# Performance work log

Measured on AMD Instinct MI355X. Metric: run time of the kernel, lower is better.

Reference implementation:

```python
import jax, jax.numpy as jnp
import numpy as np

B = 2097152   # batch
Z = 16        # z_dim
K = 64        # num_hidden_nodes


def setup_inputs() -> dict:
    key = jax.random.key(0)
    k1, k2, k3, k4, k5 = jax.random.split(key, 5)
    return {
        "z": jax.random.normal(k1, (B, Z), dtype=jnp.float32),
        "a_0": jax.random.normal(k2, (1,), dtype=jnp.float32),
        "bk": jax.random.normal(k3, (K,), dtype=jnp.float32),
        "ck": jax.random.normal(k4, (K, Z), dtype=jnp.float32),
        "dk": jax.random.normal(k5, (K,), dtype=jnp.float32),
    }


def reference(z, a_0, bk, ck, dk):
    # Vectorized over the batch: y[b] = a_0 + sum_k bk[k] * tanh((ck @ z[b])[k] + dk[k])
    h = jnp.tanh(jnp.einsum("bz,kz->bk", z, ck) + dk)  # [B, K]
    y = a_0 + h @ bk                                     # [B]
    return y[:, None]                                     # [B, 1]
```

## Files before the change

kernel.cpp:

```cpp
#include <hip/hip_runtime.h>
#include <stdint.h>

typedef __attribute__((ext_vector_type(8)))  short  short8;
typedef __attribute__((ext_vector_type(8)))  __bf16 bf16x8;
typedef __attribute__((ext_vector_type(16))) float  floatx16;
typedef __attribute__((ext_vector_type(4)))  float  floatx4;
typedef __attribute__((ext_vector_type(2)))  float  float2v;
typedef __attribute__((ext_vector_type(4)))  uint32_t uint4v;

union Frag { short8 s; bf16x8 v; uint4v d; };
union FU   { float f; uint32_t u; };

__device__ __forceinline__ short f2bf(float f) {
    FU x; x.f = f;
    uint32_t r = x.u + 0x7fffu + ((x.u >> 16) & 1u);
    return (short)(r >> 16);
}

__device__ __forceinline__ uint32_t pack_bf2(float lo, float hi) {
    FU a, b; a.f = lo; b.f = hi;
    return __builtin_amdgcn_perm(b.u + 0x8000u, a.u + 0x8000u, 0x07060302u);
}

__device__ __forceinline__ float fexp2(float x) { return __builtin_amdgcn_exp2f(x); }
__device__ __forceinline__ float frcp(float x)  { return __builtin_amdgcn_rcpf(x); }
__device__ __forceinline__ float fclamp(float x, float lo, float hi) {
#if __has_builtin(__builtin_amdgcn_fmed3f)
    return __builtin_amdgcn_fmed3f(x, lo, hi);
#else
    return fminf(fmaxf(x, lo), hi);
#endif
}

__device__ __forceinline__ float2v tpair(float a, float b) {
    float2v t;
    t.x = fexp2(fclamp(a, -30.0f, 30.0f));
    t.y = fexp2(fclamp(b, -30.0f, 30.0f));
    return t + 1.0f;
}

__global__ __launch_bounds__(256) void mave_kernel(
    const float* __restrict__ z,
    const float* __restrict__ a0,
    const float* __restrict__ bk,
    const float* __restrict__ ck,
    const float* __restrict__ dk,
    float* __restrict__ out,
    int ntiles)
{
    const int lane = threadIdx.x & 63;
    const int m    = lane & 31;
    const int g    = lane >> 5;
    const float S  = 2.885390081777927f;

    const int wid   = (int)((blockIdx.x * blockDim.x + threadIdx.x) >> 6);
    const int tile0 = wid * 8;
    if (tile0 >= ntiles) return;
    const int tlast = ntiles - 1;

    const float* zp = z + (size_t)m * 16 + g * 8;

    floatx4 zb[4][2];
    #pragma unroll
    for (int i = 0; i < 4; ++i) {
        int ti = tile0 + i; if (ti > tlast) ti = tlast;
        const float* q = zp + (size_t)ti * 512;
        zb[i][0] = *(const floatx4*)q;
        zb[i][1] = *(const floatx4*)(q + 4);
    }

    Frag af0, af1;
    {
        const float* c0 = ck + m * 16 + g * 8;
        const float* c1 = c0 + 32 * 16;
        #pragma unroll
        for (int e = 0; e < 8; ++e) {
            af0.s[e] = f2bf(c0[e] * S);
            af1.s[e] = f2bf(c1[e] * S);
        }
    }
    floatx16 cinit0, cinit1;
    float2v  nb2[16];
    #pragma unroll
    for (int r = 0; r < 16; ++r) {
        int n = (r & 3) + 8 * (r >> 2) + 4 * g;
        cinit0[r] = S * dk[n];
        cinit1[r] = S * dk[n + 32];
        nb2[r].x = -2.0f * bk[n];
        nb2[r].y = -2.0f * bk[n + 32];
    }
    float base = a0[0];
    for (int k = 0; k < 64; ++k) base += bk[k];

    float yv[8];
    #pragma unroll
    for (int i = 0; i < 8; ++i) {
        const int s4 = i & 3;

        Frag bfr;
        bfr.d[0] = pack_bf2(zb[s4][0].x, zb[s4][0].y);
        bfr.d[1] = pack_bf2(zb[s4][0].z, zb[s4][0].w);
        bfr.d[2] = pack_bf2(zb[s4][1].x, zb[s4][1].y);
        bfr.d[3] = pack_bf2(zb[s4][1].z, zb[s4][1].w);

        if (i + 4 < 8) {
            int ti = tile0 + i + 4; if (ti > tlast) ti = tlast;
            const float* q = zp + (size_t)ti * 512;
            zb[s4][0] = *(const floatx4*)q;
            zb[s4][1] = *(const floatx4*)(q + 4);
        }

        floatx16 acc0 = __builtin_amdgcn_mfma_f32_32x32x16_bf16(af0.v, bfr.v, cinit0, 0, 0, 0);
        floatx16 acc1 = __builtin_amdgcn_mfma_f32_32x32x16_bf16(af1.v, bfr.v, cinit1, 0, 0, 0);

        float2v Ya = {0.0f, 0.0f}, Yb = {0.0f, 0.0f};
        #pragma unroll
        for (int r = 0; r < 16; r += 4) {
            float2v T0 = tpair(acc0[r+0], acc1[r+0]);
            float2v T1 = tpair(acc0[r+1], acc1[r+1]);
            float2v T2 = tpair(acc0[r+2], acc1[r+2]);
            float2v T3 = tpair(acc0[r+3], acc1[r+3]);
            float2v P01 = T0 * T1, P23 = T2 * T3, P = P01 * P23;
            float2v R; R.x = frcp(P.x); R.y = frcp(P.y);
            float2v n01 = nb2[r+0] * T1 + nb2[r+1] * T0;
            float2v n23 = nb2[r+2] * T3 + nb2[r+3] * T2;
            float2v num = n01 * P23 + n23 * P01;
            if (r & 4) Yb += num * R; else Ya += num * R;
        }
        float2v Yv = Ya + Yb;
        yv[i] = Yv.x + Yv.y;
    }

    float ov[8];
    #pragma unroll
    for (int i = 0; i < 8; ++i) ov[i] = __shfl_xor(yv[i], 32, 64);
    if (g == 0) {
        #pragma unroll
        for (int i = 0; i < 8; ++i) {
            int ti = tile0 + i; if (ti > tlast) ti = tlast;
            out[(size_t)ti * 32 + m] = base + yv[i] + ov[i];
        }
    }
}

extern "C" void kernel_launch(void* const* d_in, const int* in_sizes, int n_in,
                              void* d_out, int out_size, void* d_ws, size_t ws_size,
                              hipStream_t stream) {
    const float* z  = (const float*)d_in[0];
    const float* a0 = (const float*)d_in[1];
    const float* bk = (const float*)d_in[2];
    const float* ck = (const float*)d_in[3];
    const float* dk = (const float*)d_in[4];
    float* out = (float*)d_out;

    const int B      = in_sizes[0] / 16;
    const int ntiles = B / 32;

    const int blocks = (ntiles + 31) / 32;
    hipLaunchKernelGGL(mave_kernel, dim3(blocks), dim3(256), 0, stream,
                       z, a0, bk, ck, dk, out, ntiles);
}
```

Baseline: 198.1 us.

## Stage per-block constants in LDS and process MFMA halves sequentially to cut VGPRs

Moves the dk/bk-derived accumulator inits, the -2*bk coefficient pairs and the bias sum into shared memory, computed once per block by the first wave using a shuffle reduction. Inside the loop it reloads those constants from LDS and handles the two 32-row MFMA halves one after another, pairing rows within a half rather than across halves. The z prefetch depth drops from 4 to 3 tiles. The aim is to lower register pressure to raise occupancy and to remove the redundant per-thread 64-element bias loop. The cost is a block barrier, extra LDS reads each iteration, and a shallower prefetch.

```diff
diff --git a/kernel.cpp b/kernel.cpp
--- a/kernel.cpp
+++ b/kernel.cpp
@@ -53,6 +53,32 @@
     const int g    = lane >> 5;
     const float S  = 2.885390081777927f;
 
+    __shared__ __align__(16) float   cinitL[2][2][16];
+    __shared__ __align__(16) float2v nbL[2][2][2][4];
+    __shared__ float baseL;
+
+    if (threadIdx.x < 64) {
+        const int t = threadIdx.x;
+        {
+            const int gg = t >> 5, hh = (t >> 4) & 1, r = t & 15;
+            const int n  = (r & 3) + 8 * (r >> 2) + 4 * gg + 32 * hh;
+            cinitL[gg][hh][r] = S * dk[n];
+        }
+        if (t < 32) {
+            const int gg = t >> 4, hh = (t >> 3) & 1, rg = (t >> 2) & 1, j = t & 3;
+            const int rl = 8 * rg + j,     rh = 8 * rg + 4 + j;
+            const int nl = (rl & 3) + 8 * (rl >> 2) + 4 * gg + 32 * hh;
+            const int nh = (rh & 3) + 8 * (rh >> 2) + 4 * gg + 32 * hh;
+            float2v nb; nb.x = -2.0f * bk[nl]; nb.y = -2.0f * bk[nh];
+            nbL[gg][hh][rg][j] = nb;
+        }
+        float bv = bk[t];
+        #pragma unroll
+        for (int d = 1; d < 64; d <<= 1) bv += __shfl_xor(bv, d, 64);
+        if (t == 0) baseL = a0[0] + bv;
+    }
+    __syncthreads();
+
     const int wid   = (int)((blockIdx.x * blockDim.x + threadIdx.x) >> 6);
     const int tile0 = wid * 8;
     if (tile0 >= ntiles) return;
@@ -60,77 +86,78 @@
 
     const float* zp = z + (size_t)m * 16 + g * 8;
 
-    floatx4 zb[4][2];
+    floatx4 zb[3][2];
     #pragma unroll
-    for (int i = 0; i < 4; ++i) {
+    for (int i = 0; i < 3; ++i) {
         int ti = tile0 + i; if (ti > tlast) ti = tlast;
         const float* q = zp + (size_t)ti * 512;
         zb[i][0] = *(const floatx4*)q;
         zb[i][1] = *(const floatx4*)(q + 4);
     }
 
-    Frag af0, af1;
+    Frag af[2];
     {
         const float* c0 = ck + m * 16 + g * 8;
-        const float* c1 = c0 + 32 * 16;
         #pragma unroll
         for (int e = 0; e < 8; ++e) {
-            af0.s[e] = f2bf(c0[e] * S);
-            af1.s[e] = f2bf(c1[e] * S);
+            af[0].s[e] = f2bf(c0[e] * S);
+            af[1].s[e] = f2bf(c0[32 * 16 + e] * S);
         }
     }
-    floatx16 cinit0, cinit1;
-    float2v  nb2[16];
-    #pragma unroll
-    for (int r = 0; r < 16; ++r) {
-        int n = (r & 3) + 8 * (r >> 2) + 4 * g;
-        cinit0[r] = S * dk[n];
-        cinit1[r] = S * dk[n + 32];
-        nb2[r].x = -2.0f * bk[n];
-        nb2[r].y = -2.0f * bk[n + 32];
-    }
-    float base = a0[0];
-    for (int k = 0; k < 64; ++k) base += bk[k];
+
+    const floatx4* cqg = (const floatx4*)&cinitL[g][0][0];
+    const floatx4* nqg = (const floatx4*)&nbL[g][0][0][0];
 
     float yv[8];
     #pragma unroll
     for (int i = 0; i < 8; ++i) {
-        const int s4 = i & 3;
+        const int s3 = i % 3;
 
         Frag bfr;
-        bfr.d[0] = pack_bf2(zb[s4][0].x, zb[s4][0].y);
-        bfr.d[1] = pack_bf2(zb[s4][0].z, zb[s4][0].w);
-        bfr.d[2] = pack_bf2(zb[s4][1].x, zb[s4][1].y);
-        bfr.d[3] = pack_bf2(zb[s4][1].z, zb[s4][1].w);
+        bfr.d[0] = pack_bf2(zb[s3][0].x, zb[s3][0].y);
+        bfr.d[1] = pack_bf2(zb[s3][0].z, zb[s3][0].w);
+        bfr.d[2] = pack_bf2(zb[s3][1].x, zb[s3][1].y);
+        bfr.d[3] = pack_bf2(zb[s3][1].z, zb[s3][1].w);
 
-        if (i + 4 < 8) {
-            int ti = tile0 + i + 4; if (ti > tlast) ti = tlast;
+        if (i + 3 < 8) {
+            int ti = tile0 + i + 3; if (ti > tlast) ti = tlast;
             const float* q = zp + (size_t)ti * 512;
-            zb[s4][0] = *(const floatx4*)q;
-            zb[s4][1] = *(const floatx4*)(q + 4);
+            zb[s3][0] = *(const floatx4*)q;
+            zb[s3][1] = *(const floatx4*)(q + 4);
         }
 
-        floatx16 acc0 = __builtin_amdgcn_mfma_f32_32x32x16_bf16(af0.v, bfr.v, cinit0, 0, 0, 0);
-        floatx16 acc1 = __builtin_amdgcn_mfma_f32_32x32x16_bf16(af1.v, bfr.v, cinit1, 0, 0, 0);
+        float ya = 0.0f;
+        #pragma unroll
+        for (int h = 0; h < 2; ++h) {
+            union { floatx16 v; floatx4 q[4]; } C;
+            C.q[0] = cqg[h * 4 + 0]; C.q[1] = cqg[h * 4 + 1];
+            C.q[2] = cqg[h * 4 + 2]; C.q[3] = cqg[h * 4 + 3];
+            floatx16 acc = __builtin_amdgcn_mfma_f32_32x32x16_bf16(
+                af[h].v, bfr.v, C.v, 0, 0, 0);
 
-        float2v Ya = {0.0f, 0.0f}, Yb = {0.0f, 0.0f};
-        #pragma unroll
-        for (int r = 0; r < 16; r += 4) {
-            float2v T0 = tpair(acc0[r+0], acc1[r+0]);
-            float2v T1 = tpair(acc0[r+1], acc1[r+1]);
-            float2v T2 = tpair(acc0[r+2], acc1[r+2]);
-            float2v T3 = tpair(acc0[r+3], acc1[r+3]);
-            float2v P01 = T0 * T1, P23 = T2 * T3, P = P01 * P23;
-            float2v R; R.x = frcp(P.x); R.y = frcp(P.y);
-            float2v n01 = nb2[r+0] * T1 + nb2[r+1] * T0;
-            float2v n23 = nb2[r+2] * T3 + nb2[r+3] * T2;
-            float2v num = n01 * P23 + n23 * P01;
-            if (r & 4) Yb += num * R; else Ya += num * R;
+            float2v Y = {0.0f, 0.0f};
+            #pragma unroll
+            for (int rg = 0; rg < 2; ++rg) {
+                union { floatx4 q; float2v p[2]; } NA, NB;
+                NA.q = nqg[h * 4 + rg * 2 + 0];
+                NB.q = nqg[h * 4 + rg * 2 + 1];
+                float2v T0 = tpair(acc[8 * rg + 0], acc[8 * rg + 4]);
+                float2v T1 = tpair(acc[8 * rg + 1], acc[8 * rg + 5]);
+                float2v T2 = tpair(acc[8 * rg + 2], acc[8 * rg + 6]);
+                float2v T3 = tpair(acc[8 * rg + 3], acc[8 * rg + 7]);
+                float2v P01 = T0 * T1, P23 = T2 * T3, P = P01 * P23;
+                float2v R; R.x = frcp(P.x); R.y = frcp(P.y);
+                float2v n01 = NA.p[0] * T1 + NA.p[1] * T0;
+                float2v n23 = NB.p[0] * T3 + NB.p[1] * T2;
+                float2v num = n01 * P23 + n23 * P01;
+                Y += num * R;
+            }
+            ya += Y.x + Y.y;
         }
-        float2v Yv = Ya + Yb;
-        yv[i] = Yv.x + Yv.y;
+        yv[i] = ya;
     }
 
+    const float base = baseL;
     float ov[8];
     #pragma unroll
     for (int i = 0; i < 8; ++i) ov[i] = __shfl_xor(yv[i], 32, 64);
```

Result: no change. 200.6 us (+1.3%).
